# Kernel tuning notes

Hardware: AMD Instinct MI355X
Metric: run time of the kernel (lower is better)

## Reference

```python
import jax, jax.numpy as jnp
import numpy as np

B, S, D = 2, 2048, 768
HD = 64          # hardcoded head_dim in module
NH = D // HD     # 12 query heads
NKV = max(1, NH // 3)  # 4 kv heads
GROUPS = NH // NKV     # 3
WINDOW = 384
THETA = 10000.0
EPS = 1e-6


def setup_inputs() -> dict:
    key = jax.random.key(0)
    ks = jax.random.split(key, 5)
    return {
        "hidden_states": jax.random.normal(ks[0], (B, S, D), dtype=jnp.float32),
        "q_w": jax.random.normal(ks[1], (NH * HD, D), dtype=jnp.float32) * 0.02,
        "k_w": jax.random.normal(ks[2], (NKV * HD, D), dtype=jnp.float32) * 0.02,
        "v_w": jax.random.normal(ks[3], (NKV * HD, D), dtype=jnp.float32) * 0.02,
        "o_w": jax.random.normal(ks[4], (D, NH * HD), dtype=jnp.float32) * 0.02,
        "q_ln_w": jnp.ones((HD,), dtype=jnp.float32),
        "k_ln_w": jnp.ones((HD,), dtype=jnp.float32),
    }


def _rmsnorm(x, w):
    var = jnp.mean(jnp.square(x.astype(jnp.float32)), axis=-1, keepdims=True)
    return w * (x * jax.lax.rsqrt(var + EPS)).astype(x.dtype)


def _rotate_half(x):
    x1, x2 = jnp.split(x, 2, axis=-1)
    return jnp.concatenate((-x2, x1), axis=-1)


def _rope_cos_sin(seq_len, dtype):
    inv_freq = 1.0 / (THETA ** (jnp.arange(0, HD, 2, dtype=jnp.float32) / HD))
    t = jnp.arange(seq_len, dtype=jnp.float32)
    freqs = jnp.outer(t, inv_freq)            # [S, HD/2]
    emb = jnp.concatenate((freqs, freqs), -1)  # [S, HD]
    return jnp.cos(emb).astype(dtype), jnp.sin(emb).astype(dtype)


def reference(hidden_states, q_w, k_w, v_w, o_w, q_ln_w, k_ln_w):
    b, s, _ = hidden_states.shape
    # projections (nn.Linear: y = x @ W.T)
    q = hidden_states @ q_w.T   # [B,S,NH*HD]
    k = hidden_states @ k_w.T   # [B,S,NKV*HD]
    v = hidden_states @ v_w.T

    q = _rmsnorm(q.reshape(b, s, NH, HD), q_ln_w).transpose(0, 2, 1, 3)      # [B,NH,S,HD]
    k = _rmsnorm(k.reshape(b, s, NKV, HD), k_ln_w).transpose(0, 2, 1, 3)     # [B,NKV,S,HD]
    v = v.reshape(b, s, NKV, HD).transpose(0, 2, 1, 3)                       # [B,NKV,S,HD]

    cos, sin = _rope_cos_sin(s, q.dtype)  # [S,HD]
    cos = cos[None, None]
    sin = sin[None, None]
    q = q * cos + _rotate_half(q) * sin
    k = k * cos + _rotate_half(k) * sin

    # grouped-query repeat: [B,NKV,S,HD] -> [B,NH,S,HD]
    k = jnp.repeat(k, GROUPS, axis=1)
    v = jnp.repeat(v, GROUPS, axis=1)

    scores = jnp.einsum("bhqd,bhkd->bhqk", q, k) / np.sqrt(HD)
    # causal + sliding-window mask: allow i-WINDOW < j <= i
    idx = jnp.arange(s)
    rel = idx[None, :] - idx[:, None]  # j - i
    allowed = (rel <= 0) & (rel > -WINDOW)
    scores = jnp.where(allowed[None, None], scores, -jnp.inf)

    attn = jax.nn.softmax(scores.astype(jnp.float32), axis=-1).astype(q.dtype)
    out = jnp.einsum("bhqk,bhkd->bhqd", attn, v)       # [B,NH,S,HD]
    out = out.transpose(0, 2, 1, 3).reshape(b, s, NH * HD)
    return out @ o_w.T
```

## Files before the change

kernel.cpp:

```cpp
#include <hip/hip_runtime.h>
#include <hip/hip_bf16.h>

typedef __hip_bfloat16 bf16;
typedef __attribute__((ext_vector_type(8))) short bf16x8;
typedef __attribute__((ext_vector_type(4))) float f32x4;
typedef __attribute__((ext_vector_type(16))) float f32x16;

#define MFMA16(a, b, c) __builtin_amdgcn_mfma_f32_16x16x32_bf16((a), (b), (c), 0, 0, 0)
#define MFMA32(a, b, c) __builtin_amdgcn_mfma_f32_32x32x16_bf16((a), (b), (c), 0, 0, 0)


__device__ __forceinline__ void st4bf(bf16* p, float4 v) {
    bf16 t[4];
    t[0] = __float2bfloat16(v.x); t[1] = __float2bfloat16(v.y);
    t[2] = __float2bfloat16(v.z); t[3] = __float2bfloat16(v.w);
    *reinterpret_cast<uint2*>(p) = *reinterpret_cast<const uint2*>(t);
}

__global__ __launch_bounds__(256) void k_prep(
    const float* __restrict__ hs, const float* __restrict__ qw,
    const float* __restrict__ kw, const float* __restrict__ vw,
    const float* __restrict__ ow,
    bf16* __restrict__ hsb, bf16* __restrict__ qwb, bf16* __restrict__ kwb,
    bf16* __restrict__ vwb, bf16* __restrict__ owb, float2* __restrict__ tab)
{
    const int bid = blockIdx.x, tid = threadIdx.x;
    const float* src; bf16* dst; int rel;
    if (bid < 3072)      { src = hs; dst = hsb; rel = bid; }
    else if (bid < 3648) { src = qw; dst = qwb; rel = bid - 3072; }
    else if (bid < 3840) { src = kw; dst = kwb; rel = bid - 3648; }
    else if (bid < 4032) { src = vw; dst = vwb; rel = bid - 3840; }
    else if (bid < 4608) { src = ow; dst = owb; rel = bid - 4032; }
    else {
        int i = (bid - 4608) * 256 + tid;
        int f = i & 31;
        float ang = (float)(i >> 5) * expf(-(float)f * 0.28782313662425572f);
        float sn, cs; sincosf(ang, &sn, &cs);
        tab[i] = make_float2(cs, sn);
        return;
    }
    int i = (rel * 256 + tid) * 4;
    float4 v = *reinterpret_cast<const float4*>(src + i);
    st4bf(dst + i, v);
}

__global__ __launch_bounds__(256) void k_qkv(
    const bf16* __restrict__ hsb, const bf16* __restrict__ qwb,
    const bf16* __restrict__ kwb, const bf16* __restrict__ vwb,
    const float* __restrict__ qln, const float* __restrict__ kln,
    const float2* __restrict__ tab,
    bf16* __restrict__ qo, bf16* __restrict__ ko, bf16* __restrict__ vto)
{
    __shared__ bf16 As[2][64 * 72];
    __shared__ bf16 Bs[2][64 * 72];
    const int tid = threadIdx.x;
    const int w = tid >> 6, l = tid & 63;
    const int lm = l & 15, lg = l >> 4;
    const int m0 = blockIdx.x * 64;
    const int nblk = blockIdx.y;

    const bf16* wsrc; int wrow0, kind, head;
    if (nblk < 12)      { wsrc = qwb; wrow0 = nblk * 64;        kind = 0; head = nblk; }
    else if (nblk < 16) { wsrc = kwb; wrow0 = (nblk - 12) * 64; kind = 1; head = nblk - 12; }
    else                { wsrc = vwb; wrow0 = (nblk - 16) * 64; kind = 2; head = nblk - 16; }

    const int sr = tid >> 2, sc = (tid & 3) * 16;
    const bf16* aptr = hsb  + (size_t)(m0 + sr) * 768 + sc;
    const bf16* bptr = wsrc + (size_t)(wrow0 + sr) * 768 + sc;

    bf16x8 ra0 = *(const bf16x8*)(aptr);
    bf16x8 ra1 = *(const bf16x8*)(aptr + 8);
    bf16x8 rb0 = *(const bf16x8*)(bptr);
    bf16x8 rb1 = *(const bf16x8*)(bptr + 8);

    f32x4 acc[4] = {};
    for (int t = 0; t < 12; ++t) {
        const int p = t & 1;
        *(bf16x8*)(&As[p][sr * 72 + sc])     = ra0;
        *(bf16x8*)(&As[p][sr * 72 + sc + 8]) = ra1;
        *(bf16x8*)(&Bs[p][sr * 72 + sc])     = rb0;
        *(bf16x8*)(&Bs[p][sr * 72 + sc + 8]) = rb1;
        __syncthreads();
        if (t < 11) {
            const int off = (t + 1) * 64;
            ra0 = *(const bf16x8*)(aptr + off);
            ra1 = *(const bf16x8*)(aptr + off + 8);
            rb0 = *(const bf16x8*)(bptr + off);
            rb1 = *(const bf16x8*)(bptr + off + 8);
        }
        #pragma unroll
        for (int kk = 0; kk < 2; ++kk) {
            bf16x8 af = *(const bf16x8*)(&As[p][(w * 16 + lm) * 72 + kk * 32 + lg * 8]);
            #pragma unroll
            for (int ct = 0; ct < 4; ++ct) {
                bf16x8 bfr = *(const bf16x8*)(&Bs[p][(ct * 16 + lm) * 72 + kk * 32 + lg * 8]);
                acc[ct] = MFMA16(af, bfr, acc[ct]);
            }
        }
    }

    const int b  = m0 >> 11;
    const int s0 = m0 & 2047;

    if (kind == 2) {
        bf16* base = vto + (size_t)(b * 4 + head) * 64 * 2048;
        #pragma unroll
        for (int r = 0; r < 4; ++r) {
            const int s = s0 + w * 16 + lg * 4 + r;
            #pragma unroll
            for (int ct = 0; ct < 4; ++ct)
                base[(size_t)(ct * 16 + lm) * 2048 + s] = __float2bfloat16(acc[ct][r]);
        }
        return;
    }

    const float* ln = (kind == 0) ? qln : kln;
    const float qscl = (kind == 0) ? 0.18033688011117042f : 1.0f;
    float lw[4];
    #pragma unroll
    for (int ct = 0; ct < 4; ++ct) lw[ct] = ln[ct * 16 + lm] * qscl;

    bf16* base = (kind == 0) ? qo + ((size_t)(b * 12 + head) * 2048 + s0) * 64
                             : ko + ((size_t)(b * 4  + head) * 2048 + s0) * 64;
    #pragma unroll
    for (int r = 0; r < 4; ++r) {
        float n0 = acc[0][r], n1 = acc[1][r], n2 = acc[2][r], n3 = acc[3][r];
        float ss = n0 * n0 + n1 * n1 + n2 * n2 + n3 * n3;
        ss += __shfl_xor(ss, 1);
        ss += __shfl_xor(ss, 2);
        ss += __shfl_xor(ss, 4);
        ss += __shfl_xor(ss, 8);
        float rms = rsqrtf(ss * (1.0f / 64.0f) + 1e-6f);
        n0 *= rms * lw[0]; n1 *= rms * lw[1]; n2 *= rms * lw[2]; n3 *= rms * lw[3];
        const int row = w * 16 + lg * 4 + r;
        const float2* tp = tab + (size_t)(s0 + row) * 32;
        float2 t0 = tp[lm], t1 = tp[lm + 16];
        bf16* dst = base + (size_t)row * 64;
        dst[lm]      = __float2bfloat16(n0 * t0.x - n2 * t0.y);
        dst[lm + 16] = __float2bfloat16(n1 * t1.x - n3 * t1.y);
        dst[lm + 32] = __float2bfloat16(n2 * t0.x + n0 * t0.y);
        dst[lm + 48] = __float2bfloat16(n3 * t1.x + n1 * t1.y);
    }
}

__global__ __launch_bounds__(128) void k_attn(
    const bf16* __restrict__ qi, const bf16* __restrict__ ki,
    const bf16* __restrict__ vti, bf16* __restrict__ ao)
{
    __shared__ bf16 Ks[2][64 * 72];
    __shared__ bf16 Vs[2][64 * 72];
    const int tid = threadIdx.x;
    const int w = tid >> 6, l = tid & 63;
    const int p = l >> 5, c31 = l & 31;
    const int qb = blockIdx.x, h = blockIdx.y, b = blockIdx.z;
    const int kv = h / 3;
    const int q0 = qb * 64;
    const int qw0 = q0 + w * 32;
    const int q_g = qw0 + c31;

    const bf16* qrow = qi + ((size_t)((b * 12 + h) * 2048 + q_g)) * 64 + p * 8;
    bf16x8 qf0 = *(const bf16x8*)(qrow);
    bf16x8 qf1 = *(const bf16x8*)(qrow + 16);
    bf16x8 qf2 = *(const bf16x8*)(qrow + 32);
    bf16x8 qf3 = *(const bf16x8*)(qrow + 48);

    f32x16 oacc0 = {}, oacc1 = {};
    float m_ = -INFINITY, l_ = 0.f;

    const int sr = tid >> 1, sc = (tid & 1) * 32;
    const bf16* kgb = ki  + (size_t)(b * 4 + kv) * 2048 * 64;
    const bf16* vgb = vti + (size_t)(b * 4 + kv) * 64 * 2048;

    const int kb_lo = (qb > 6) ? (qb - 6) : 0;
    bf16x8 rk[4], rv[4];
    {
        const bf16* kp = kgb + (size_t)(kb_lo * 64 + sr) * 64 + sc;
        const bf16* vp = vgb + (size_t)sr * 2048 + kb_lo * 64 + sc;
        #pragma unroll
        for (int j = 0; j < 4; ++j) {
            rk[j] = *(const bf16x8*)(kp + j * 8);
            rv[j] = *(const bf16x8*)(vp + j * 8);
        }
    }

    for (int kb = kb_lo; kb <= qb; ++kb) {
        const int pb = (kb - kb_lo) & 1;
        const int k0 = kb * 64;

        #pragma unroll
        for (int j = 0; j < 4; ++j) {
            *(bf16x8*)(&Ks[pb][sr * 72 + sc + j * 8]) = rk[j];
            *(bf16x8*)(&Vs[pb][sr * 72 + sc + j * 8]) = rv[j];
        }
        __syncthreads();
        if (kb < qb) {
            const bf16* kp = kgb + (size_t)(k0 + 64 + sr) * 64 + sc;
            const bf16* vp = vgb + (size_t)sr * 2048 + k0 + 64 + sc;
            #pragma unroll
            for (int j = 0; j < 4; ++j) {
                rk[j] = *(const bf16x8*)(kp + j * 8);
                rv[j] = *(const bf16x8*)(vp + j * 8);
            }
        }

        f32x16 s0 = {}, s1 = {};
        {
            const bf16* kbase = &Ks[pb][c31 * 72 + p * 8];
            s0 = MFMA32(*(const bf16x8*)(kbase),      qf0, s0);
            s0 = MFMA32(*(const bf16x8*)(kbase + 16), qf1, s0);
            s0 = MFMA32(*(const bf16x8*)(kbase + 32), qf2, s0);
            s0 = MFMA32(*(const bf16x8*)(kbase + 48), qf3, s0);
            const bf16* kbase1 = kbase + 32 * 72;
            s1 = MFMA32(*(const bf16x8*)(kbase1),      qf0, s1);
            s1 = MFMA32(*(const bf16x8*)(kbase1 + 16), qf1, s1);
            s1 = MFMA32(*(const bf16x8*)(kbase1 + 32), qf2, s1);
            s1 = MFMA32(*(const bf16x8*)(kbase1 + 48), qf3, s1);
        }

        const bool need_mask = (64 * kb + 63 > qw0) || (64 * kb <= qw0 - 353);
        if (need_mask) {
            #pragma unroll
            for (int r = 0; r < 16; ++r) {
                int kl = (r & 3) + 8 * (r >> 2) + 4 * p;
                int kg0 = k0 + kl, kg1 = k0 + 32 + kl;
                bool ok0 = (kg0 <= q_g) && (kg0 > q_g - 384);
                bool ok1 = (kg1 <= q_g) && (kg1 > q_g - 384);
                s0[r] = ok0 ? s0[r] : -INFINITY;
                s1[r] = ok1 ? s1[r] : -INFINITY;
            }
        }

        float tmax = s0[0];
        #pragma unroll
        for (int r = 1; r < 16; ++r) tmax = fmaxf(tmax, s0[r]);
        #pragma unroll
        for (int r = 0; r < 16; ++r) tmax = fmaxf(tmax, s1[r]);
        tmax = fmaxf(tmax, __shfl_xor(tmax, 32));

        float mnew = fmaxf(m_, tmax);
        float scale, rs = 0.f;
        if (mnew > -INFINITY) {
            scale = exp2f(m_ - mnew);
            #pragma unroll
            for (int r = 0; r < 16; ++r) { s0[r] = exp2f(s0[r] - mnew); rs += s0[r]; }
            #pragma unroll
            for (int r = 0; r < 16; ++r) { s1[r] = exp2f(s1[r] - mnew); rs += s1[r]; }
        } else {
            scale = 1.f;
            #pragma unroll
            for (int r = 0; r < 16; ++r) { s0[r] = 0.f; s1[r] = 0.f; }
        }
        m_ = mnew;
        rs += __shfl_xor(rs, 32);
        l_ = l_ * scale + rs;
        #pragma unroll
        for (int r = 0; r < 16; ++r) { oacc0[r] *= scale; oacc1[r] *= scale; }

        bf16x8 paf[4];
        #pragma unroll
        for (int kt = 0; kt < 2; ++kt) {
            unsigned pk[8];
            #pragma unroll
            for (int i = 0; i < 8; ++i) {
                float lo = (kt == 0) ? s0[2 * i] : s1[2 * i];
                float hi = (kt == 0) ? s0[2 * i + 1] : s1[2 * i + 1];
                bf16 blo = __float2bfloat16(lo), bhi = __float2bfloat16(hi);
                pk[i] = ((unsigned)*(unsigned short*)&bhi << 16) | (unsigned)*(unsigned short*)&blo;
            }
            unsigned x[8];
            #pragma unroll
            for (int i = 0; i < 8; ++i) x[i] = (unsigned)__shfl_xor((int)pk[i], 32);
            #pragma unroll
            for (int s = 0; s < 2; ++s) {
                union { int4 i4; bf16x8 v; } u;
                u.i4.x = p ? (int)x[4 * s + 2] : (int)pk[4 * s];
                u.i4.y = p ? (int)x[4 * s + 3] : (int)pk[4 * s + 1];
                u.i4.z = p ? (int)pk[4 * s + 2] : (int)x[4 * s];
                u.i4.w = p ? (int)pk[4 * s + 3] : (int)x[4 * s + 1];
                paf[kt * 2 + s] = u.v;
            }
        }

        {
            const bf16* vbase = &Vs[pb][c31 * 72 + p * 8];
            oacc0 = MFMA32(*(const bf16x8*)(vbase),      paf[0], oacc0);
            oacc0 = MFMA32(*(const bf16x8*)(vbase + 16), paf[1], oacc0);
            oacc0 = MFMA32(*(const bf16x8*)(vbase + 32), paf[2], oacc0);
            oacc0 = MFMA32(*(const bf16x8*)(vbase + 48), paf[3], oacc0);
            const bf16* vbase1 = vbase + 32 * 72;
            oacc1 = MFMA32(*(const bf16x8*)(vbase1),      paf[0], oacc1);
            oacc1 = MFMA32(*(const bf16x8*)(vbase1 + 16), paf[1], oacc1);
            oacc1 = MFMA32(*(const bf16x8*)(vbase1 + 32), paf[2], oacc1);
            oacc1 = MFMA32(*(const bf16x8*)(vbase1 + 48), paf[3], oacc1);
        }
        __syncthreads();
    }

    const float inv = 1.f / l_;
    bf16* dst = ao + ((size_t)(b * 2048 + q_g)) * 768 + h * 64;
    #pragma unroll
    for (int g = 0; g < 4; ++g) {
        union { uint2 u2; bf16 t[4]; } o0, o1;
        #pragma unroll
        for (int e = 0; e < 4; ++e) {
            o0.t[e] = __float2bfloat16(oacc0[4 * g + e] * inv);
            o1.t[e] = __float2bfloat16(oacc1[4 * g + e] * inv);
        }
        *reinterpret_cast<uint2*>(dst + 8 * g + 4 * p)      = o0.u2;
        *reinterpret_cast<uint2*>(dst + 32 + 8 * g + 4 * p) = o1.u2;
    }
}

__global__ __launch_bounds__(256) void k_oproj(
    const bf16* __restrict__ A, const bf16* __restrict__ W, float* __restrict__ out)
{
    __shared__ bf16 As[2][64 * 72];
    __shared__ bf16 Bs[2][64 * 72];
    const int tid = threadIdx.x;
    const int w = tid >> 6, l = tid & 63;
    const int lm = l & 15, lg = l >> 4;
    const int m0 = blockIdx.x * 64, n0 = blockIdx.y * 64;

    const int sr = tid >> 2, sc = (tid & 3) * 16;
    const bf16* aptr = A + (size_t)(m0 + sr) * 768 + sc;
    const bf16* bptr = W + (size_t)(n0 + sr) * 768 + sc;

    bf16x8 ra0 = *(const bf16x8*)(aptr);
    bf16x8 ra1 = *(const bf16x8*)(aptr + 8);
    bf16x8 rb0 = *(const bf16x8*)(bptr);
    bf16x8 rb1 = *(const bf16x8*)(bptr + 8);

    f32x4 acc[4] = {};
    for (int t = 0; t < 12; ++t) {
        const int p = t & 1;
        *(bf16x8*)(&As[p][sr * 72 + sc])     = ra0;
        *(bf16x8*)(&As[p][sr * 72 + sc + 8]) = ra1;
        *(bf16x8*)(&Bs[p][sr * 72 + sc])     = rb0;
        *(bf16x8*)(&Bs[p][sr * 72 + sc + 8]) = rb1;
        __syncthreads();
        if (t < 11) {
            const int off = (t + 1) * 64;
            ra0 = *(const bf16x8*)(aptr + off);
            ra1 = *(const bf16x8*)(aptr + off + 8);
            rb0 = *(const bf16x8*)(bptr + off);
            rb1 = *(const bf16x8*)(bptr + off + 8);
        }
        #pragma unroll
        for (int kk = 0; kk < 2; ++kk) {
            bf16x8 af = *(const bf16x8*)(&As[p][(w * 16 + lm) * 72 + kk * 32 + lg * 8]);
            #pragma unroll
            for (int ct = 0; ct < 4; ++ct) {
                bf16x8 bfr = *(const bf16x8*)(&Bs[p][(ct * 16 + lm) * 72 + kk * 32 + lg * 8]);
                acc[ct] = MFMA16(af, bfr, acc[ct]);
            }
        }
    }

    #pragma unroll
    for (int r = 0; r < 4; ++r) {
        float* dst = out + (size_t)(m0 + w * 16 + lg * 4 + r) * 768 + n0;
        #pragma unroll
        for (int ct = 0; ct < 4; ++ct)
            dst[ct * 16 + lm] = acc[ct][r];
    }
}

extern "C" void kernel_launch(void* const* d_in, const int* in_sizes, int n_in,
                              void* d_out, int out_size, void* d_ws, size_t ws_size,
                              hipStream_t stream) {
    const float* hs  = (const float*)d_in[0];
    const float* qw  = (const float*)d_in[1];
    const float* kw  = (const float*)d_in[2];
    const float* vw  = (const float*)d_in[3];
    const float* ow  = (const float*)d_in[4];
    const float* qln = (const float*)d_in[5];
    const float* kln = (const float*)d_in[6];
    float* out = (float*)d_out;

    float2* tab  = (float2*)d_ws;
    bf16*   q_ws = (bf16*)(tab + 65536);
    bf16*   k_ws = q_ws + 3145728;
    bf16*   vt_ws= k_ws + 1048576;
    bf16*   x_ws = vt_ws + 1048576;
    bf16*   qwb  = x_ws + 3145728;
    bf16*   kwb  = qwb + 589824;
    bf16*   vwb  = kwb + 196608;
    bf16*   owb  = vwb + 196608;

    k_prep<<<dim3(4864), 256, 0, stream>>>(hs, qw, kw, vw, ow, x_ws, qwb, kwb, vwb, owb, tab);
    k_qkv<<<dim3(64, 20, 1), 256, 0, stream>>>(x_ws, qwb, kwb, vwb, qln, kln, tab, q_ws, k_ws, vt_ws);
    k_attn<<<dim3(32, 12, 2), 128, 0, stream>>>(q_ws, k_ws, vt_ws, x_ws);
    k_oproj<<<dim3(64, 12, 1), 256, 0, stream>>>(x_ws, owb, out);
}
```

Before: 68.22 us.

## Use direct global-to-LDS loads and 128-row tiles in projection GEMMs

Replaces the register-staged LDS fills in the QKV and output-projection GEMMs with global_load_lds 16-byte transfers into a fragment-ordered LDS layout, so each lane reads its MFMA operand contiguously. It also doubles the M tile to 128 rows, with two fragments per wave, to raise B-operand reuse, and halves the grid. The aim is to cut VGPR round-trips and LDS write instructions. In exchange the grid drops to 640 and 384 blocks, which may underfill the GPU, and the direct-to-LDS path needs correct wait and synchronization semantics.

```diff
diff --git a/kernel.cpp b/kernel.cpp
--- a/kernel.cpp
+++ b/kernel.cpp
@@ -9,6 +9,12 @@
 #define MFMA16(a, b, c) __builtin_amdgcn_mfma_f32_16x16x32_bf16((a), (b), (c), 0, 0, 0)
 #define MFMA32(a, b, c) __builtin_amdgcn_mfma_f32_32x32x16_bf16((a), (b), (c), 0, 0, 0)
 
+
+__device__ __forceinline__ void gload16(const bf16* g, bf16* lds) {
+    __builtin_amdgcn_global_load_lds(
+        (const __attribute__((address_space(1))) void*)g,
+        (__attribute__((address_space(3))) void*)lds, 16, 0, 0);
+}
 
 __device__ __forceinline__ void st4bf(bf16* p, float4 v) {
     bf16 t[4];
@@ -51,12 +57,12 @@
     const float2* __restrict__ tab,
     bf16* __restrict__ qo, bf16* __restrict__ ko, bf16* __restrict__ vto)
 {
-    __shared__ bf16 As[2][64 * 72];
-    __shared__ bf16 Bs[2][64 * 72];
+    __shared__ bf16 As[2][16 * 512];
+    __shared__ bf16 Bs[2][8 * 512];
     const int tid = threadIdx.x;
     const int w = tid >> 6, l = tid & 63;
     const int lm = l & 15, lg = l >> 4;
-    const int m0 = blockIdx.x * 64;
+    const int m0 = blockIdx.x * 128;
     const int nblk = blockIdx.y;
 
     const bf16* wsrc; int wrow0, kind, head;
@@ -64,38 +70,44 @@
     else if (nblk < 16) { wsrc = kwb; wrow0 = (nblk - 12) * 64; kind = 1; head = nblk - 12; }
     else                { wsrc = vwb; wrow0 = (nblk - 16) * 64; kind = 2; head = nblk - 16; }
 
-    const int sr = tid >> 2, sc = (tid & 3) * 16;
-    const bf16* aptr = hsb  + (size_t)(m0 + sr) * 768 + sc;
-    const bf16* bptr = wsrc + (size_t)(wrow0 + sr) * 768 + sc;
-
-    bf16x8 ra0 = *(const bf16x8*)(aptr);
-    bf16x8 ra1 = *(const bf16x8*)(aptr + 8);
-    bf16x8 rb0 = *(const bf16x8*)(bptr);
-    bf16x8 rb1 = *(const bf16x8*)(bptr + 8);
-
-    f32x4 acc[4] = {};
+    const bf16* asrc = hsb  + (size_t)(m0 + w * 32 + lm) * 768 + lg * 8;
+    const bf16* bsrc = wsrc + (size_t)(wrow0 + lm) * 768 + lg * 8;
+
+    auto stage = [&](int pb, int k0) {
+        #pragma unroll
+        for (int mf = 0; mf < 2; ++mf)
+            #pragma unroll
+            for (int kk = 0; kk < 2; ++kk)
+                gload16(asrc + (size_t)(mf * 16) * 768 + k0 + kk * 32,
+                        &As[pb][((w * 2 + mf) * 2 + kk) * 512]);
+        #pragma unroll
+        for (int j = 0; j < 2; ++j) {
+            const int idx = w * 2 + j, kk = idx >> 2, ct = idx & 3;
+            gload16(bsrc + (size_t)(ct * 16) * 768 + k0 + kk * 32,
+                    &Bs[pb][idx * 512]);
+        }
+    };
+
+    stage(0, 0);
+    f32x4 acc[2][4] = {};
     for (int t = 0; t < 12; ++t) {
         const int p = t & 1;
-        *(bf16x8*)(&As[p][sr * 72 + sc])     = ra0;
-        *(bf16x8*)(&As[p][sr * 72 + sc + 8]) = ra1;
-        *(bf16x8*)(&Bs[p][sr * 72 + sc])     = rb0;
-        *(bf16x8*)(&Bs[p][sr * 72 + sc + 8]) = rb1;
         __syncthreads();
-        if (t < 11) {
-            const int off = (t + 1) * 64;
-            ra0 = *(const bf16x8*)(aptr + off);
-            ra1 = *(const bf16x8*)(aptr + off + 8);
-            rb0 = *(const bf16x8*)(bptr + off);
-            rb1 = *(const bf16x8*)(bptr + off + 8);
-        }
+        if (t < 11) stage(p ^ 1, (t + 1) * 64);
         #pragma unroll
         for (int kk = 0; kk < 2; ++kk) {
-            bf16x8 af = *(const bf16x8*)(&As[p][(w * 16 + lm) * 72 + kk * 32 + lg * 8]);
-            #pragma unroll
-            for (int ct = 0; ct < 4; ++ct) {
-                bf16x8 bfr = *(const bf16x8*)(&Bs[p][(ct * 16 + lm) * 72 + kk * 32 + lg * 8]);
-                acc[ct] = MFMA16(af, bfr, acc[ct]);
-            }
+            bf16x8 af[2], bfv[4];
+            #pragma unroll
+            for (int mf = 0; mf < 2; ++mf)
+                af[mf] = *(const bf16x8*)(&As[p][((w * 2 + mf) * 2 + kk) * 512 + l * 8]);
+            #pragma unroll
+            for (int ct = 0; ct < 4; ++ct)
+                bfv[ct] = *(const bf16x8*)(&Bs[p][(kk * 4 + ct) * 512 + l * 8]);
+            #pragma unroll
+            for (int mf = 0; mf < 2; ++mf)
+                #pragma unroll
+                for (int ct = 0; ct < 4; ++ct)
+                    acc[mf][ct] = MFMA16(af[mf], bfv[ct], acc[mf][ct]);
         }
     }
 
@@ -105,12 +117,14 @@
     if (kind == 2) {
         bf16* base = vto + (size_t)(b * 4 + head) * 64 * 2048;
         #pragma unroll
-        for (int r = 0; r < 4; ++r) {
-            const int s = s0 + w * 16 + lg * 4 + r;
-            #pragma unroll
-            for (int ct = 0; ct < 4; ++ct)
-                base[(size_t)(ct * 16 + lm) * 2048 + s] = __float2bfloat16(acc[ct][r]);
-        }
+        for (int mf = 0; mf < 2; ++mf)
+            #pragma unroll
+            for (int r = 0; r < 4; ++r) {
+                const int s = s0 + w * 32 + mf * 16 + lg * 4 + r;
+                #pragma unroll
+                for (int ct = 0; ct < 4; ++ct)
+                    base[(size_t)(ct * 16 + lm) * 2048 + s] = __float2bfloat16(acc[mf][ct][r]);
+            }
         return;
     }
 
@@ -123,24 +137,26 @@
     bf16* base = (kind == 0) ? qo + ((size_t)(b * 12 + head) * 2048 + s0) * 64
                              : ko + ((size_t)(b * 4  + head) * 2048 + s0) * 64;
     #pragma unroll
-    for (int r = 0; r < 4; ++r) {
-        float n0 = acc[0][r], n1 = acc[1][r], n2 = acc[2][r], n3 = acc[3][r];
-        float ss = n0 * n0 + n1 * n1 + n2 * n2 + n3 * n3;
-        ss += __shfl_xor(ss, 1);
-        ss += __shfl_xor(ss, 2);
-        ss += __shfl_xor(ss, 4);
-        ss += __shfl_xor(ss, 8);
-        float rms = rsqrtf(ss * (1.0f / 64.0f) + 1e-6f);
-        n0 *= rms * lw[0]; n1 *= rms * lw[1]; n2 *= rms * lw[2]; n3 *= rms * lw[3];
-        const int row = w * 16 + lg * 4 + r;
-        const float2* tp = tab + (size_t)(s0 + row) * 32;
-        float2 t0 = tp[lm], t1 = tp[lm + 16];
-        bf16* dst = base + (size_t)row * 64;
-        dst[lm]      = __float2bfloat16(n0 * t0.x - n2 * t0.y);
-        dst[lm + 16] = __float2bfloat16(n1 * t1.x - n3 * t1.y);
-        dst[lm + 32] = __float2bfloat16(n2 * t0.x + n0 * t0.y);
-        dst[lm + 48] = __float2bfloat16(n3 * t1.x + n1 * t1.y);
-    }
+    for (int mf = 0; mf < 2; ++mf)
+        #pragma unroll
+        for (int r = 0; r < 4; ++r) {
+            float n0 = acc[mf][0][r], n1 = acc[mf][1][r], n2 = acc[mf][2][r], n3 = acc[mf][3][r];
+            float ss = n0 * n0 + n1 * n1 + n2 * n2 + n3 * n3;
+            ss += __shfl_xor(ss, 1);
+            ss += __shfl_xor(ss, 2);
+            ss += __shfl_xor(ss, 4);
+            ss += __shfl_xor(ss, 8);
+            float rms = rsqrtf(ss * (1.0f / 64.0f) + 1e-6f);
+            n0 *= rms * lw[0]; n1 *= rms * lw[1]; n2 *= rms * lw[2]; n3 *= rms * lw[3];
+            const int row = w * 32 + mf * 16 + lg * 4 + r;
+            const float2* tp = tab + (size_t)(s0 + row) * 32;
+            float2 t0 = tp[lm], t1 = tp[lm + 16];
+            bf16* dst = base + (size_t)row * 64;
+            dst[lm]      = __float2bfloat16(n0 * t0.x - n2 * t0.y);
+            dst[lm + 16] = __float2bfloat16(n1 * t1.x - n3 * t1.y);
+            dst[lm + 32] = __float2bfloat16(n2 * t0.x + n0 * t0.y);
+            dst[lm + 48] = __float2bfloat16(n3 * t1.x + n1 * t1.y);
+        }
 }
 
 __global__ __launch_bounds__(128) void k_attn(
@@ -314,55 +330,63 @@
 __global__ __launch_bounds__(256) void k_oproj(
     const bf16* __restrict__ A, const bf16* __restrict__ W, float* __restrict__ out)
 {
-    __shared__ bf16 As[2][64 * 72];
-    __shared__ bf16 Bs[2][64 * 72];
+    __shared__ bf16 As[2][16 * 512];
+    __shared__ bf16 Bs[2][8 * 512];
     const int tid = threadIdx.x;
     const int w = tid >> 6, l = tid & 63;
     const int lm = l & 15, lg = l >> 4;
-    const int m0 = blockIdx.x * 64, n0 = blockIdx.y * 64;
-
-    const int sr = tid >> 2, sc = (tid & 3) * 16;
-    const bf16* aptr = A + (size_t)(m0 + sr) * 768 + sc;
-    const bf16* bptr = W + (size_t)(n0 + sr) * 768 + sc;
-
-    bf16x8 ra0 = *(const bf16x8*)(aptr);
-    bf16x8 ra1 = *(const bf16x8*)(aptr + 8);
-    bf16x8 rb0 = *(const bf16x8*)(bptr);
-    bf16x8 rb1 = *(const bf16x8*)(bptr + 8);
-
-    f32x4 acc[4] = {};
+    const int m0 = blockIdx.x * 128, n0 = blockIdx.y * 64;
+
+    const bf16* asrc = A + (size_t)(m0 + w * 32 + lm) * 768 + lg * 8;
+    const bf16* bsrc = W + (size_t)(n0 + lm) * 768 + lg * 8;
+
+    auto stage = [&](int pb, int k0) {
+        #pragma unroll
+        for (int mf = 0; mf < 2; ++mf)
+            #pragma unroll
+            for (int kk = 0; kk < 2; ++kk)
+                gload16(asrc + (size_t)(mf * 16) * 768 + k0 + kk * 32,
+                        &As[pb][((w * 2 + mf) * 2 + kk) * 512]);
+        #pragma unroll
+        for (int j = 0; j < 2; ++j) {
+            const int idx = w * 2 + j, kk = idx >> 2, ct = idx & 3;
+            gload16(bsrc + (size_t)(ct * 16) * 768 + k0 + kk * 32,
+                    &Bs[pb][idx * 512]);
+        }
+    };
+
+    stage(0, 0);
+    f32x4 acc[2][4] = {};
     for (int t = 0; t < 12; ++t) {
         const int p = t & 1;
-        *(bf16x8*)(&As[p][sr * 72 + sc])     = ra0;
-        *(bf16x8*)(&As[p][sr * 72 + sc + 8]) = ra1;
-        *(bf16x8*)(&Bs[p][sr * 72 + sc])     = rb0;
-        *(bf16x8*)(&Bs[p][sr * 72 + sc + 8]) = rb1;
         __syncthreads();
-        if (t < 11) {
-            const int off = (t + 1) * 64;
-            ra0 = *(const bf16x8*)(aptr + off);
-            ra1 = *(const bf16x8*)(aptr + off + 8);
-            rb0 = *(const bf16x8*)(bptr + off);
-            rb1 = *(const bf16x8*)(bptr + off + 8);
-        }
+        if (t < 11) stage(p ^ 1, (t + 1) * 64);
         #pragma unroll
         for (int kk = 0; kk < 2; ++kk) {
-            bf16x8 af = *(const bf16x8*)(&As[p][(w * 16 + lm) * 72 + kk * 32 + lg * 8]);
-            #pragma unroll
-            for (int ct = 0; ct < 4; ++ct) {
-                bf16x8 bfr = *(const bf16x8*)(&Bs[p][(ct * 16 + lm) * 72 + kk * 32 + lg * 8]);
-                acc[ct] = MFMA16(af, bfr, acc[ct]);
-            }
+            bf16x8 af[2], bfv[4];
+            #pragma unroll
+            for (int mf = 0; mf < 2; ++mf)
+                af[mf] = *(const bf16x8*)(&As[p][((w * 2 + mf) * 2 + kk) * 512 + l * 8]);
+            #pragma unroll
+            for (int ct = 0; ct < 4; ++ct)
+                bfv[ct] = *(const bf16x8*)(&Bs[p][(kk * 4 + ct) * 512 + l * 8]);
+            #pragma unroll
+            for (int mf = 0; mf < 2; ++mf)
+                #pragma unroll
+                for (int ct = 0; ct < 4; ++ct)
+                    acc[mf][ct] = MFMA16(af[mf], bfv[ct], acc[mf][ct]);
         }
     }
 
     #pragma unroll
-    for (int r = 0; r < 4; ++r) {
-        float* dst = out + (size_t)(m0 + w * 16 + lg * 4 + r) * 768 + n0;
-        #pragma unroll
-        for (int ct = 0; ct < 4; ++ct)
-            dst[ct * 16 + lm] = acc[ct][r];
-    }
+    for (int mf = 0; mf < 2; ++mf)
+        #pragma unroll
+        for (int r = 0; r < 4; ++r) {
+            float* dst = out + (size_t)(m0 + w * 32 + mf * 16 + lg * 4 + r) * 768 + n0;
+            #pragma unroll
+            for (int ct = 0; ct < 4; ++ct)
+                dst[ct * 16 + lm] = acc[mf][ct][r];
+        }
 }
 
 extern "C" void kernel_launch(void* const* d_in, const int* in_sizes, int n_in,
@@ -388,7 +412,7 @@
     bf16*   owb  = vwb + 196608;
 
     k_prep<<<dim3(4864), 256, 0, stream>>>(hs, qw, kw, vw, ow, x_ws, qwb, kwb, vwb, owb, tab);
-    k_qkv<<<dim3(64, 20, 1), 256, 0, stream>>>(x_ws, qwb, kwb, vwb, qln, kln, tab, q_ws, k_ws, vt_ws);
+    k_qkv<<<dim3(32, 20, 1), 256, 0, stream>>>(x_ws, qwb, kwb, vwb, qln, kln, tab, q_ws, k_ws, vt_ws);
     k_attn<<<dim3(32, 12, 2), 128, 0, stream>>>(q_ws, k_ws, vt_ws, x_ws);
-    k_oproj<<<dim3(64, 12, 1), 256, 0, stream>>>(x_ws, owb, out);
-}
+    k_oproj<<<dim3(32, 12, 1), 256, 0, stream>>>(x_ws, owb, out);
+}
```

Measured after the change: 84.20 us. 23.4% more time.
